# Optimization experiments

Hardware: AMD Instinct MI355X
Metric: run time of the kernel (lower is better)

Reference implementation:

```python
import jax, jax.numpy as jnp
import numpy as np

N_NODES = 50000
N_EDGES = 800000
D_FEAT = 64
IN_DIM = 1 + 2 * D_FEAT  # 129
FC_DIMS = [128, 64, 1]


def setup_inputs() -> dict:
    key = jax.random.key(0)
    ks = jax.random.split(key, 10)
    x = jax.random.normal(ks[0], (N_NODES, D_FEAT), dtype=jnp.float32)
    edge_index = jax.random.randint(ks[1], (2, N_EDGES), 0, N_NODES, dtype=jnp.int64)
    edge_weight = jax.random.uniform(ks[2], (N_EDGES, 1), dtype=jnp.float32)
    # MLP params (Linear: y = x @ W.T + b), Kaiming-ish scale
    dims = [IN_DIM] + FC_DIMS
    W1 = jax.random.normal(ks[3], (dims[1], dims[0]), dtype=jnp.float32) / np.sqrt(dims[0])
    b1 = jnp.zeros((dims[1],), dtype=jnp.float32)
    W2 = jax.random.normal(ks[4], (dims[2], dims[1]), dtype=jnp.float32) / np.sqrt(dims[1])
    b2 = jnp.zeros((dims[2],), dtype=jnp.float32)
    W3 = jax.random.normal(ks[5], (dims[3], dims[2]), dtype=jnp.float32) / np.sqrt(dims[2])
    b3 = jnp.zeros((dims[3],), dtype=jnp.float32)
    return {"x": x, "edge_index": edge_index, "edge_weight": edge_weight,
            "W1": W1, "b1": b1, "W2": W2, "b2": b2, "W3": W3, "b3": b3}


def reference(x, edge_index, edge_weight, W1, b1, W2, b2, W3, b3):
    # Gather source/target node features per edge: [E, d]
    src = x[edge_index[0]]
    tgt = x[edge_index[1]]
    # Concat [edge_weight | src | tgt] -> [E, 1 + 2d]
    h = jnp.concatenate([edge_weight, src, tgt], axis=1)
    # MLP (dropout is None / eval; last layer dim==1 -> no ReLU)
    h = jax.nn.relu(h @ W1.T + b1)
    h = jax.nn.relu(h @ W2.T + b2)
    return h @ W3.T + b3  # [E, 1] new edge weights
```

## Files before the change

### kernel.cpp

```cpp
#include <hip/hip_runtime.h>

typedef _Float16 half8 __attribute__((ext_vector_type(8)));
typedef _Float16 half4_t __attribute__((ext_vector_type(4)));
typedef float floatx4 __attribute__((ext_vector_type(4)));

__global__ __launch_bounds__(256) void prep_kernel(
    const float* __restrict__ x,
    const float* __restrict__ W1, const float* __restrict__ W2,
    const float* __restrict__ b1, const float* __restrict__ b2,
    const float* __restrict__ W3,
    _Float16* __restrict__ w2f, float* __restrict__ pf,
    _Float16* __restrict__ c0h,
    _Float16* __restrict__ Ps, _Float16* __restrict__ Pt,
    int n_nodes, int nb_gemm)
{
    const int b = blockIdx.x;
    const int tid = threadIdx.x;

    if (b < nb_gemm) {
        __shared__ __align__(16) _Float16 sW[16384];
        for (int c = tid; c < 4096; c += 256) {
            int lin = c * 4;
            int n = lin >> 7, kk = lin & 127;
            const float* wp = W1 + n * 129 + 1 + kk;
            float w0 = wp[0], w1 = wp[1], w2 = wp[2], w3 = wp[3];
            int mt = n >> 4, kb = kk >> 5;
            int L = (n & 15) + (((kk >> 3) & 3) << 4);
            int pos = (mt * 4 + kb) * 512 + L * 8 + (kk & 7);
            half4_t h = {(_Float16)w0, (_Float16)w1, (_Float16)w2, (_Float16)w3};
            *(half4_t*)(&sW[pos]) = h;
        }
        __syncthreads();

        const int lane = tid & 63, wave = tid >> 6;
        const int lrow = lane & 15, quad = lane >> 4;
        const int tile = b * 4 + wave;
        if (tile * 16 < n_nodes) {
            int node = tile * 16 + lrow;
            if (node >= n_nodes) node = n_nodes - 1;
            const float* xr = x + (size_t)node * 64 + quad * 8;
            float4 x0 = *(const float4*)(xr);
            float4 x1 = *(const float4*)(xr + 4);
            float4 x2 = *(const float4*)(xr + 32);
            float4 x3 = *(const float4*)(xr + 36);
            half8 bx0 = {(_Float16)x0.x, (_Float16)x0.y, (_Float16)x0.z, (_Float16)x0.w,
                         (_Float16)x1.x, (_Float16)x1.y, (_Float16)x1.z, (_Float16)x1.w};
            half8 bx1 = {(_Float16)x2.x, (_Float16)x2.y, (_Float16)x2.z, (_Float16)x2.w,
                         (_Float16)x3.x, (_Float16)x3.y, (_Float16)x3.z, (_Float16)x3.w};
#pragma unroll
            for (int mt = 0; mt < 8; ++mt) {
                half8 a0 = *(const half8*)(&sW[(mt * 4 + 0) * 512 + lane * 8]);
                half8 a1 = *(const half8*)(&sW[(mt * 4 + 1) * 512 + lane * 8]);
                half8 a2 = *(const half8*)(&sW[(mt * 4 + 2) * 512 + lane * 8]);
                half8 a3 = *(const half8*)(&sW[(mt * 4 + 3) * 512 + lane * 8]);
                floatx4 ap = {0.f, 0.f, 0.f, 0.f};
                floatx4 at = {0.f, 0.f, 0.f, 0.f};
                ap = __builtin_amdgcn_mfma_f32_16x16x32_f16(a0, bx0, ap, 0, 0, 0);
                ap = __builtin_amdgcn_mfma_f32_16x16x32_f16(a1, bx1, ap, 0, 0, 0);
                at = __builtin_amdgcn_mfma_f32_16x16x32_f16(a2, bx0, at, 0, 0, 0);
                at = __builtin_amdgcn_mfma_f32_16x16x32_f16(a3, bx1, at, 0, 0, 0);
                int nb = mt * 16 + quad * 4;
                float4 b1v = *(const float4*)(b1 + nb);
                half4_t hs, ht;
                hs[0] = (_Float16)(ap[0] + b1v.x);
                hs[1] = (_Float16)(ap[1] + b1v.y);
                hs[2] = (_Float16)(ap[2] + b1v.z);
                hs[3] = (_Float16)(ap[3] + b1v.w);
                ht[0] = (_Float16)at[0];
                ht[1] = (_Float16)at[1];
                ht[2] = (_Float16)at[2];
                ht[3] = (_Float16)at[3];
                *(half4_t*)(Ps + (size_t)node * 128 + nb) = hs;
                *(half4_t*)(Pt + (size_t)node * 128 + nb) = ht;
            }
        }
    } else if (b < nb_gemm + 32) {
        int t = (b - nb_gemm) * 256 + tid;
        if (t < 8192) {
            int c = t >> 9, r = t & 511;
            int L = r >> 3, jj = r & 7;
            int it = c >> 2, kb = c & 3;
            int i = it * 16 + (L & 15);
            int j = kb * 32 + (L >> 4) * 8 + jj;
            w2f[t] = (_Float16)W2[i * 128 + j];
        }
    } else {
        if (tid < 64)            pf[tid] = b2[tid];
        else if (tid < 128)      pf[tid] = W3[tid - 64];
        else                     c0h[tid - 128] = (_Float16)W1[(tid - 128) * 129];
    }
}

__global__ __launch_bounds__(256, 4) void edge_mlp_kernel(
    const _Float16* __restrict__ Ps, const _Float16* __restrict__ Pt,
    const int* __restrict__ ei, const float* __restrict__ ew,
    const float* __restrict__ b3,
    const _Float16* __restrict__ w2f, const float* __restrict__ pf,
    const _Float16* __restrict__ c0h,
    float* __restrict__ out, int E)
{
    const int tid  = threadIdx.x;
    const int lane = tid & 63;
    const int wave = tid >> 6;
    const int lrow = lane & 15;
    const int quad = lane >> 4;
    const int e0 = blockIdx.x * 128 + wave * 32;

    half8 c0f[4];
#pragma unroll
    for (int kb = 0; kb < 4; ++kb)
        c0f[kb] = *(const half8*)(c0h + kb * 32 + quad * 8);

    half8 bfr[2][4];
#pragma unroll
    for (int nt = 0; nt < 2; ++nt) {
        int e = e0 + nt * 16 + lrow; if (e >= E) e = E - 1;
        float ewf = ew[e];
        int sn = ei[e];
        int tn = ei[E + e];
        const _Float16* psp = Ps + (size_t)sn * 128 + quad * 8;
        const _Float16* ptp = Pt + (size_t)tn * 128 + quad * 8;
        _Float16 eh = (_Float16)ewf;
        half8 ev = {eh, eh, eh, eh, eh, eh, eh, eh};
        half8 z  = {0, 0, 0, 0, 0, 0, 0, 0};
#pragma unroll
        for (int kb = 0; kb < 4; ++kb) {
            half8 ps = *(const half8*)(psp + kb * 32);
            half8 pt = *(const half8*)(ptp + kb * 32);
            half8 s = ps + pt;
            s = s + ev * c0f[kb];
            s = __builtin_elementwise_max(s, z);
            bfr[nt][kb] = s;
        }
    }

    const float b3v = b3[0];
    float tot0 = b3v, tot1 = b3v;
#pragma unroll
    for (int it = 0; it < 4; ++it) {
        half8 a2[4];
#pragma unroll
        for (int kb = 0; kb < 4; ++kb)
            a2[kb] = *(const half8*)(w2f + (it * 4 + kb) * 512 + lane * 8);
        int ib = it * 16 + quad * 4;
        float4 b2v = *(const float4*)(pf + ib);
        float4 w3v = *(const float4*)(pf + 64 + ib);
#pragma unroll
        for (int nt = 0; nt < 2; ++nt) {
            floatx4 a = {0.f, 0.f, 0.f, 0.f};
#pragma unroll
            for (int kb = 0; kb < 4; ++kb)
                a = __builtin_amdgcn_mfma_f32_16x16x32_f16(a2[kb], bfr[nt][kb], a, 0, 0, 0);
            float p = fmaxf(a[0] + b2v.x, 0.f) * w3v.x;
            p      += fmaxf(a[1] + b2v.y, 0.f) * w3v.y;
            p      += fmaxf(a[2] + b2v.z, 0.f) * w3v.z;
            p      += fmaxf(a[3] + b2v.w, 0.f) * w3v.w;
            p += __shfl_xor(p, 16, 64);
            p += __shfl_xor(p, 32, 64);
            if (nt == 0) tot0 += p; else tot1 += p;
        }
    }

    if (quad == 0) {
        int oe0 = e0 + lrow;
        int oe1 = e0 + 16 + lrow;
        if (oe0 < E) out[oe0] = tot0;
        if (oe1 < E) out[oe1] = tot1;
    }
}

extern "C" void kernel_launch(void* const* d_in, const int* in_sizes, int n_in,
                              void* d_out, int out_size, void* d_ws, size_t ws_size,
                              hipStream_t stream) {
    const float* x  = (const float*)d_in[0];
    const int*   ei = (const int*)d_in[1];
    const float* ew = (const float*)d_in[2];
    const float* W1 = (const float*)d_in[3];
    const float* b1 = (const float*)d_in[4];
    const float* W2 = (const float*)d_in[5];
    const float* b2 = (const float*)d_in[6];
    const float* W3 = (const float*)d_in[7];
    const float* b3 = (const float*)d_in[8];
    float* out = (float*)d_out;
    const int E = in_sizes[2];
    const int n_x = in_sizes[0];
    const int n_nodes = n_x / 64;

    _Float16* w2f = (_Float16*)d_ws;
    float*    pf  = (float*)((char*)d_ws + 16384);
    _Float16* c0h = (_Float16*)((char*)d_ws + 16896);
    _Float16* Ps  = (_Float16*)((char*)d_ws + 17152);
    _Float16* Pt  = (_Float16*)((char*)d_ws + 17152 + (size_t)n_nodes * 256);

    int tiles = (n_nodes + 15) / 16;
    int nb_gemm = (tiles + 3) / 4;
    prep_kernel<<<nb_gemm + 33, 256, 0, stream>>>(x, W1, W2, b1, b2, W3,
                                                  w2f, pf, c0h, Ps, Pt,
                                                  n_nodes, nb_gemm);

    int nblk = (E + 127) / 128;
    edge_mlp_kernel<<<nblk, 256, 0, stream>>>(Ps, Pt, ei, ew, b3,
                                              w2f, pf, c0h, out, E);
}
```

Measured before the change: 159.8 us.

## Pre-swizzle W1 once, stage W2 into LDS asynchronously, hoist edge index loads

W1 is now converted and swizzled once by a separate prep kernel instead of by every GEMM block, so the node GEMM blocks only copy a ready fp16 layout into shared memory. The edge kernel loads the W2 fragments into LDS with global_load_lds, issued early so the copy overlaps the gathers, and reads them from LDS instead of global memory. Edge indices and weights for both sub-tiles are loaded up front to raise memory-level parallelism. In exchange there is one extra kernel launch, a block-wide barrier in the edge kernel, and 16KB of LDS per block, which may limit occupancy.

```diff
diff --git a/kernel.cpp b/kernel.cpp
--- a/kernel.cpp
+++ b/kernel.cpp
@@ -4,90 +4,90 @@
 typedef _Float16 half4_t __attribute__((ext_vector_type(4)));
 typedef float floatx4 __attribute__((ext_vector_type(4)));
 
-__global__ __launch_bounds__(256) void prep_kernel(
-    const float* __restrict__ x,
+__global__ __launch_bounds__(256) void prep1_kernel(
     const float* __restrict__ W1, const float* __restrict__ W2,
-    const float* __restrict__ b1, const float* __restrict__ b2,
-    const float* __restrict__ W3,
-    _Float16* __restrict__ w2f, float* __restrict__ pf,
-    _Float16* __restrict__ c0h,
-    _Float16* __restrict__ Ps, _Float16* __restrict__ Pt,
-    int n_nodes, int nb_gemm)
+    const float* __restrict__ b2, const float* __restrict__ W3,
+    _Float16* __restrict__ wsh, float* __restrict__ pf, _Float16* __restrict__ c0h)
 {
-    const int b = blockIdx.x;
-    const int tid = threadIdx.x;
-
-    if (b < nb_gemm) {
-        __shared__ __align__(16) _Float16 sW[16384];
-        for (int c = tid; c < 4096; c += 256) {
-            int lin = c * 4;
-            int n = lin >> 7, kk = lin & 127;
-            const float* wp = W1 + n * 129 + 1 + kk;
-            float w0 = wp[0], w1 = wp[1], w2 = wp[2], w3 = wp[3];
-            int mt = n >> 4, kb = kk >> 5;
-            int L = (n & 15) + (((kk >> 3) & 3) << 4);
-            int pos = (mt * 4 + kb) * 512 + L * 8 + (kk & 7);
-            half4_t h = {(_Float16)w0, (_Float16)w1, (_Float16)w2, (_Float16)w3};
-            *(half4_t*)(&sW[pos]) = h;
-        }
-        __syncthreads();
-
-        const int lane = tid & 63, wave = tid >> 6;
-        const int lrow = lane & 15, quad = lane >> 4;
-        const int tile = b * 4 + wave;
-        if (tile * 16 < n_nodes) {
-            int node = tile * 16 + lrow;
-            if (node >= n_nodes) node = n_nodes - 1;
-            const float* xr = x + (size_t)node * 64 + quad * 8;
-            float4 x0 = *(const float4*)(xr);
-            float4 x1 = *(const float4*)(xr + 4);
-            float4 x2 = *(const float4*)(xr + 32);
-            float4 x3 = *(const float4*)(xr + 36);
-            half8 bx0 = {(_Float16)x0.x, (_Float16)x0.y, (_Float16)x0.z, (_Float16)x0.w,
-                         (_Float16)x1.x, (_Float16)x1.y, (_Float16)x1.z, (_Float16)x1.w};
-            half8 bx1 = {(_Float16)x2.x, (_Float16)x2.y, (_Float16)x2.z, (_Float16)x2.w,
-                         (_Float16)x3.x, (_Float16)x3.y, (_Float16)x3.z, (_Float16)x3.w};
-#pragma unroll
-            for (int mt = 0; mt < 8; ++mt) {
-                half8 a0 = *(const half8*)(&sW[(mt * 4 + 0) * 512 + lane * 8]);
-                half8 a1 = *(const half8*)(&sW[(mt * 4 + 1) * 512 + lane * 8]);
-                half8 a2 = *(const half8*)(&sW[(mt * 4 + 2) * 512 + lane * 8]);
-                half8 a3 = *(const half8*)(&sW[(mt * 4 + 3) * 512 + lane * 8]);
-                floatx4 ap = {0.f, 0.f, 0.f, 0.f};
-                floatx4 at = {0.f, 0.f, 0.f, 0.f};
-                ap = __builtin_amdgcn_mfma_f32_16x16x32_f16(a0, bx0, ap, 0, 0, 0);
-                ap = __builtin_amdgcn_mfma_f32_16x16x32_f16(a1, bx1, ap, 0, 0, 0);
-                at = __builtin_amdgcn_mfma_f32_16x16x32_f16(a2, bx0, at, 0, 0, 0);
-                at = __builtin_amdgcn_mfma_f32_16x16x32_f16(a3, bx1, at, 0, 0, 0);
-                int nb = mt * 16 + quad * 4;
-                float4 b1v = *(const float4*)(b1 + nb);
-                half4_t hs, ht;
-                hs[0] = (_Float16)(ap[0] + b1v.x);
-                hs[1] = (_Float16)(ap[1] + b1v.y);
-                hs[2] = (_Float16)(ap[2] + b1v.z);
-                hs[3] = (_Float16)(ap[3] + b1v.w);
-                ht[0] = (_Float16)at[0];
-                ht[1] = (_Float16)at[1];
-                ht[2] = (_Float16)at[2];
-                ht[3] = (_Float16)at[3];
-                *(half4_t*)(Ps + (size_t)node * 128 + nb) = hs;
-                *(half4_t*)(Pt + (size_t)node * 128 + nb) = ht;
-            }
-        }
-    } else if (b < nb_gemm + 32) {
-        int t = (b - nb_gemm) * 256 + tid;
-        if (t < 8192) {
+    int b = blockIdx.x;
+    if (b < 96) {
+        int tid = b * 256 + threadIdx.x;
+        if (tid < 16384) {
+            int c = tid >> 9, r = tid & 511;
+            int L = r >> 3, jj = r & 7;
+            int mt = c >> 2, kb = c & 3;
+            int n = mt * 16 + (L & 15);
+            int k = kb * 32 + (L >> 4) * 8 + jj;
+            wsh[tid] = (_Float16)W1[n * 129 + 1 + k];
+        } else {
+            int t = tid - 16384;
             int c = t >> 9, r = t & 511;
             int L = r >> 3, jj = r & 7;
             int it = c >> 2, kb = c & 3;
             int i = it * 16 + (L & 15);
             int j = kb * 32 + (L >> 4) * 8 + jj;
-            w2f[t] = (_Float16)W2[i * 128 + j];
+            wsh[tid] = (_Float16)W2[i * 128 + j];
         }
     } else {
-        if (tid < 64)            pf[tid] = b2[tid];
-        else if (tid < 128)      pf[tid] = W3[tid - 64];
-        else                     c0h[tid - 128] = (_Float16)W1[(tid - 128) * 129];
+        int tid = threadIdx.x;
+        if (tid < 64)        pf[tid] = b2[tid];
+        else if (tid < 128)  pf[tid] = W3[tid - 64];
+        else                 c0h[tid - 128] = (_Float16)W1[(tid - 128) * 129];
+    }
+}
+
+__global__ __launch_bounds__(256) void prep2_kernel(
+    const float* __restrict__ x, const float* __restrict__ b1,
+    const _Float16* __restrict__ wsh,
+    _Float16* __restrict__ Ps, _Float16* __restrict__ Pt, int n_nodes)
+{
+    __shared__ __align__(16) _Float16 sW[16384];
+    const int tid = threadIdx.x;
+    for (int c = tid; c < 2048; c += 256)
+        *(half8*)(&sW[c * 8]) = *(const half8*)(wsh + c * 8);
+    __syncthreads();
+
+    const int lane = tid & 63, wave = tid >> 6;
+    const int lrow = lane & 15, quad = lane >> 4;
+    const int tile = blockIdx.x * 4 + wave;
+    if (tile * 16 >= n_nodes) return;
+    int node = tile * 16 + lrow;
+    if (node >= n_nodes) node = n_nodes - 1;
+
+    const float* xr = x + (size_t)node * 64 + quad * 8;
+    float4 x0 = *(const float4*)(xr);
+    float4 x1 = *(const float4*)(xr + 4);
+    float4 x2 = *(const float4*)(xr + 32);
+    float4 x3 = *(const float4*)(xr + 36);
+    half8 bx0 = {(_Float16)x0.x, (_Float16)x0.y, (_Float16)x0.z, (_Float16)x0.w,
+                 (_Float16)x1.x, (_Float16)x1.y, (_Float16)x1.z, (_Float16)x1.w};
+    half8 bx1 = {(_Float16)x2.x, (_Float16)x2.y, (_Float16)x2.z, (_Float16)x2.w,
+                 (_Float16)x3.x, (_Float16)x3.y, (_Float16)x3.z, (_Float16)x3.w};
+#pragma unroll
+    for (int mt = 0; mt < 8; ++mt) {
+        half8 a0 = *(const half8*)(&sW[(mt * 4 + 0) * 512 + lane * 8]);
+        half8 a1 = *(const half8*)(&sW[(mt * 4 + 1) * 512 + lane * 8]);
+        half8 a2 = *(const half8*)(&sW[(mt * 4 + 2) * 512 + lane * 8]);
+        half8 a3 = *(const half8*)(&sW[(mt * 4 + 3) * 512 + lane * 8]);
+        floatx4 ap = {0.f, 0.f, 0.f, 0.f};
+        floatx4 at = {0.f, 0.f, 0.f, 0.f};
+        ap = __builtin_amdgcn_mfma_f32_16x16x32_f16(a0, bx0, ap, 0, 0, 0);
+        ap = __builtin_amdgcn_mfma_f32_16x16x32_f16(a1, bx1, ap, 0, 0, 0);
+        at = __builtin_amdgcn_mfma_f32_16x16x32_f16(a2, bx0, at, 0, 0, 0);
+        at = __builtin_amdgcn_mfma_f32_16x16x32_f16(a3, bx1, at, 0, 0, 0);
+        int nb = mt * 16 + quad * 4;
+        float4 b1v = *(const float4*)(b1 + nb);
+        half4_t hs, ht;
+        hs[0] = (_Float16)(ap[0] + b1v.x);
+        hs[1] = (_Float16)(ap[1] + b1v.y);
+        hs[2] = (_Float16)(ap[2] + b1v.z);
+        hs[3] = (_Float16)(ap[3] + b1v.w);
+        ht[0] = (_Float16)at[0];
+        ht[1] = (_Float16)at[1];
+        ht[2] = (_Float16)at[2];
+        ht[3] = (_Float16)at[3];
+        *(half4_t*)(Ps + (size_t)node * 128 + nb) = hs;
+        *(half4_t*)(Pt + (size_t)node * 128 + nb) = ht;
     }
 }
 
@@ -99,6 +99,8 @@
     const _Float16* __restrict__ c0h,
     float* __restrict__ out, int E)
 {
+    __shared__ __align__(16) _Float16 sW2[8192];
+
     const int tid  = threadIdx.x;
     const int lane = tid & 63;
     const int wave = tid >> 6;
@@ -106,6 +108,21 @@
     const int quad = lane >> 4;
     const int e0 = blockIdx.x * 128 + wave * 32;
 
+    int e_a = e0 + lrow;      if (e_a >= E) e_a = E - 1;
+    int e_b = e0 + 16 + lrow; if (e_b >= E) e_b = E - 1;
+    int sn0 = ei[e_a], tn0 = ei[E + e_a];
+    int sn1 = ei[e_b], tn1 = ei[E + e_b];
+    float ew0 = ew[e_a], ew1 = ew[e_b];
+
+#pragma unroll
+    for (int i = 0; i < 4; ++i) {
+        const _Float16* g = w2f + wave * 2048 + i * 512 + lane * 8;
+        __builtin_amdgcn_global_load_lds(
+            (const __attribute__((address_space(1))) void*)g,
+            (__attribute__((address_space(3))) void*)&sW2[wave * 2048 + i * 512],
+            16, 0, 0);
+    }
+
     half8 c0f[4];
 #pragma unroll
     for (int kb = 0; kb < 4; ++kb)
@@ -114,10 +131,9 @@
     half8 bfr[2][4];
 #pragma unroll
     for (int nt = 0; nt < 2; ++nt) {
-        int e = e0 + nt * 16 + lrow; if (e >= E) e = E - 1;
-        float ewf = ew[e];
-        int sn = ei[e];
-        int tn = ei[E + e];
+        int sn = nt ? sn1 : sn0;
+        int tn = nt ? tn1 : tn0;
+        float ewf = nt ? ew1 : ew0;
         const _Float16* psp = Ps + (size_t)sn * 128 + quad * 8;
         const _Float16* ptp = Pt + (size_t)tn * 128 + quad * 8;
         _Float16 eh = (_Float16)ewf;
@@ -134,6 +150,8 @@
         }
     }
 
+    __syncthreads();
+
     const float b3v = b3[0];
     float tot0 = b3v, tot1 = b3v;
 #pragma unroll
@@ -141,7 +159,7 @@
         half8 a2[4];
 #pragma unroll
         for (int kb = 0; kb < 4; ++kb)
-            a2[kb] = *(const half8*)(w2f + (it * 4 + kb) * 512 + lane * 8);
+            a2[kb] = *(const half8*)(&sW2[(it * 4 + kb) * 512 + lane * 8]);
         int ib = it * 16 + quad * 4;
         float4 b2v = *(const float4*)(pf + ib);
         float4 w3v = *(const float4*)(pf + 64 + ib);
@@ -186,19 +204,19 @@
     const int n_x = in_sizes[0];
     const int n_nodes = n_x / 64;
 
-    _Float16* w2f = (_Float16*)d_ws;
-    float*    pf  = (float*)((char*)d_ws + 16384);
-    _Float16* c0h = (_Float16*)((char*)d_ws + 16896);
-    _Float16* Ps  = (_Float16*)((char*)d_ws + 17152);
-    _Float16* Pt  = (_Float16*)((char*)d_ws + 17152 + (size_t)n_nodes * 256);
+    _Float16* wsh = (_Float16*)d_ws;
+    float*    pf  = (float*)((char*)d_ws + 49152);
+    _Float16* c0h = (_Float16*)((char*)d_ws + 49664);
+    _Float16* Ps  = (_Float16*)((char*)d_ws + 49920);
+    _Float16* Pt  = (_Float16*)((char*)d_ws + 49920 + (size_t)n_nodes * 256);
+
+    prep1_kernel<<<97, 256, 0, stream>>>(W1, W2, b2, W3, wsh, pf, c0h);
 
     int tiles = (n_nodes + 15) / 16;
-    int nb_gemm = (tiles + 3) / 4;
-    prep_kernel<<<nb_gemm + 33, 256, 0, stream>>>(x, W1, W2, b1, b2, W3,
-                                                  w2f, pf, c0h, Ps, Pt,
-                                                  n_nodes, nb_gemm);
+    int nb2 = (tiles + 3) / 4;
+    prep2_kernel<<<nb2, 256, 0, stream>>>(x, b1, wsh, Ps, Pt, n_nodes);
 
     int nblk = (E + 127) / 128;
     edge_mlp_kernel<<<nblk, 256, 0, stream>>>(Ps, Pt, ei, ew, b3,
-                                              w2f, pf, c0h, out, E);
-}
+                                              wsh + 16384, pf, c0h, out, E);
+}
```

Measured after the change: 151.6 us. -5.1%, faster.
